# Optimization experiments

Measured on AMD Instinct MI355X. Metric: run time of the kernel, lower is better.

The kernel has to match this reference:

```python
import jax, jax.numpy as jnp
import numpy as np

BATCH = 65536
IN_FEATURES = 128
OUT_FEATURES = 128
GRID = 8  # initial_grid: number of RBF/spline basis centers per edge


def setup_inputs() -> dict:
    key = jax.random.key(0)
    k1, k2, k3 = jax.random.split(key, 3)
    x = jax.random.normal(k1, (BATCH, IN_FEATURES), dtype=jnp.float32)
    # Per-edge spline coefficients stacked: [out, in, grid]
    coeffs = jax.random.normal(k2, (OUT_FEATURES, IN_FEATURES, GRID), dtype=jnp.float32) * 0.1
    # Per-edge base (SiLU) weights stacked: [out, in]
    base_w = jax.random.normal(k3, (OUT_FEATURES, IN_FEATURES), dtype=jnp.float32) * 0.1
    # Shared uniform grid of RBF centers in [-1, 1]
    centers = jnp.linspace(-1.0, 1.0, GRID, dtype=jnp.float32)
    return {"x": x, "coeffs": coeffs, "base_w": base_w, "centers": centers}


def reference(x, coeffs, base_w, centers):
    # HybridBasisFunction per edge: base_w * silu(x) + sum_g coeffs[g] * exp(-((x-c_g)/w)^2)
    width = 2.0 / (GRID - 1)  # grid spacing
    # basis: [B, in, G]
    diff = (x[:, :, None] - centers[None, None, :]) / width
    basis = jnp.exp(-diff * diff)
    # Sum over all edges (j -> i): output[b, i] = sum_j phi_ij(x[b, j])
    out = jnp.einsum('big,oig->bo', basis, coeffs)
    out = out + jnp.einsum('bi,oi->bo', jax.nn.silu(x), base_w)
    return out
```

## Files before the change

### kernel.cpp

```cpp
#include <hip/hip_runtime.h>

typedef __fp16   pk16x2 __attribute__((ext_vector_type(2)));
typedef _Float16 f16x8  __attribute__((ext_vector_type(8)));
typedef float    f32x4  __attribute__((ext_vector_type(4)));
typedef float    f32x16 __attribute__((ext_vector_type(16)));

#define BATCH 65536
#define NIN   128
#define NOUT  128

#define L2E   1.4426950408889634f
#define SQL2E 1.2011224087864498f
#define EM2   0.1353352832366127f


__global__ __launch_bounds__(256) void kan_prep(const float* __restrict__ coeffs,
                                                const float* __restrict__ base_w,
                                                _Float16* __restrict__ W3) {
    int t = blockIdx.x * 256 + threadIdx.x;
    int ks   = t >> 8;
    int c    = t & 255;
    int nbb  = c >> 6;
    int lane = c & 63;
    int sub  = lane >> 5;
    int col  = nbb * 32 + (lane & 31);
    f16x8 v;
    if (ks < 64) {
        int g = ks >> 3, t2 = ks & 7;
        const float* src = coeffs + ((size_t)col * 128 + g * 16 + sub * 8 + t2) * 8;
#pragma unroll
        for (int e = 0; e < 8; ++e) v[e] = (_Float16)src[e];
    } else {
        const float* src = base_w + (size_t)col * 128 + (ks - 64) * 16 + sub * 8;
#pragma unroll
        for (int e = 0; e < 8; ++e) v[e] = (_Float16)src[e];
    }
    *(f16x8*)((char*)W3 + (size_t)t * 16) = v;
}

__device__ __forceinline__ void gll16(const void* g, void* l) {
    __builtin_amdgcn_global_load_lds(
        (const __attribute__((address_space(1))) unsigned int*)g,
        (__attribute__((address_space(3))) unsigned int*)l, 16, 0, 0);
}

__device__ __forceinline__ f16x8 basis8r(float t) {
    float u  = t * SQL2E;
    float b0 = __builtin_amdgcn_exp2f(-(u * u));
    float r  = __builtin_amdgcn_exp2f(__builtin_fmaf(t, 2.0f * L2E, -L2E));
    float b1 = b0 * r; r *= EM2;
    float b2 = b1 * r; r *= EM2;
    float b3 = b2 * r; r *= EM2;
    float b4 = b3 * r; r *= EM2;
    float b5 = b4 * r; r *= EM2;
    float b6 = b5 * r; r *= EM2;
    float b7 = b6 * r;
    pk16x2 p0 = __builtin_amdgcn_cvt_pkrtz(b0, b1);
    pk16x2 p1 = __builtin_amdgcn_cvt_pkrtz(b2, b3);
    pk16x2 p2 = __builtin_amdgcn_cvt_pkrtz(b4, b5);
    pk16x2 p3 = __builtin_amdgcn_cvt_pkrtz(b6, b7);
    f16x8 o;
    o[0] = p0[0]; o[1] = p0[1]; o[2] = p1[0]; o[3] = p1[1];
    o[4] = p2[0]; o[5] = p2[1]; o[6] = p3[0]; o[7] = p3[1];
    return o;
}

__device__ __forceinline__ float silu1(float xv) {
    float p = __builtin_amdgcn_exp2f(-xv * L2E);
    return xv * __builtin_amdgcn_rcpf(1.0f + p);
}

__global__ __launch_bounds__(256, 2) void kan_main(const float* __restrict__ x,
                                                   const float* __restrict__ centers,
                                                   const _Float16* __restrict__ W3,
                                                   float* __restrict__ out) {
    __shared__ _Float16 smem[2][16384];

    const int tid  = threadIdx.x;
    const int lane = tid & 63;
    const int w    = tid >> 6;
    const int l31  = lane & 31;
    const int sub  = lane >> 5;
    const int row0 = blockIdx.x * 128 + w * 32;

    const float* xp = x + (size_t)(row0 + l31) * NIN;

    f32x16 acc[4];
#pragma unroll
    for (int nbb = 0; nbb < 4; ++nbb)
#pragma unroll
        for (int r = 0; r < 16; ++r) acc[nbb][r] = 0.f;

    const char* wbase = (const char*)W3;
#define STAGE(buf, grp)                                                         \
    do {                                                                        \
        const char* _s = wbase + (size_t)(grp) * 32768 + (size_t)tid * 16;      \
        char*       _d = (char*)&smem[(buf)][0] + (size_t)tid * 16;             \
        _Pragma("unroll")                                                       \
        for (int _i = 0; _i < 8; ++_i) gll16(_s + _i * 4096, _d + _i * 4096);   \
    } while (0)

    STAGE(0, 0);
    f32x4 xa = *(const f32x4*)(xp + sub * 8);
    f32x4 xb = *(const f32x4*)(xp + sub * 8 + 4);
    __syncthreads();

#pragma unroll
    for (int g = 0; g < 8; ++g) {
        const int cur = g & 1;
        STAGE(cur ^ 1, g + 1);
        const int nxt = (g < 7) ? (g + 1) * 16 : 0;
        f32x4 xa2 = *(const f32x4*)(xp + nxt + sub * 8);
        f32x4 xb2 = *(const f32x4*)(xp + nxt + sub * 8 + 4);

        f16x8 a[8];
#pragma unroll
        for (int t2 = 0; t2 < 4; ++t2) a[t2]     = basis8r(__builtin_fmaf(xa[t2], 3.5f, 3.5f));
#pragma unroll
        for (int t2 = 0; t2 < 4; ++t2) a[4 + t2] = basis8r(__builtin_fmaf(xb[t2], 3.5f, 3.5f));

#pragma unroll
        for (int t2 = 0; t2 < 8; ++t2) {
            const char* bp = (const char*)&smem[cur][0] + t2 * 4096 + lane * 16;
#pragma unroll
            for (int nbb = 0; nbb < 4; ++nbb) {
                f16x8 b = *(const f16x8*)(bp + nbb * 1024);
                acc[nbb] = __builtin_amdgcn_mfma_f32_32x32x16_f16(a[t2], b, acc[nbb], 0, 0, 0);
            }
        }
        xa = xa2; xb = xb2;
        __syncthreads();
    }

#pragma unroll
    for (int s = 0; s < 8; ++s) {
        f32x4 xa2, xb2;
        if (s < 7) {
            xa2 = *(const f32x4*)(xp + (s + 1) * 16 + sub * 8);
            xb2 = *(const f32x4*)(xp + (s + 1) * 16 + sub * 8 + 4);
        }
        float s0 = silu1(xa[0]), s1 = silu1(xa[1]), s2 = silu1(xa[2]), s3 = silu1(xa[3]);
        float s4 = silu1(xb[0]), s5 = silu1(xb[1]), s6 = silu1(xb[2]), s7 = silu1(xb[3]);
        pk16x2 p0 = __builtin_amdgcn_cvt_pkrtz(s0, s1);
        pk16x2 p1 = __builtin_amdgcn_cvt_pkrtz(s2, s3);
        pk16x2 p2 = __builtin_amdgcn_cvt_pkrtz(s4, s5);
        pk16x2 p3 = __builtin_amdgcn_cvt_pkrtz(s6, s7);
        f16x8 a;
        a[0] = p0[0]; a[1] = p0[1]; a[2] = p1[0]; a[3] = p1[1];
        a[4] = p2[0]; a[5] = p2[1]; a[6] = p3[0]; a[7] = p3[1];
        const char* bp = (const char*)&smem[0][0] + s * 4096 + lane * 16;
#pragma unroll
        for (int nbb = 0; nbb < 4; ++nbb) {
            f16x8 b = *(const f16x8*)(bp + nbb * 1024);
            acc[nbb] = __builtin_amdgcn_mfma_f32_32x32x16_f16(a, b, acc[nbb], 0, 0, 0);
        }
        if (s < 7) { xa = xa2; xb = xb2; }
    }

#pragma unroll
    for (int nbb = 0; nbb < 4; ++nbb)
#pragma unroll
        for (int r = 0; r < 16; ++r) {
            int crow = (r & 3) + 8 * (r >> 2) + 4 * sub;
            out[(size_t)(row0 + crow) * NOUT + nbb * 32 + l31] = acc[nbb][r];
        }
}

extern "C" void kernel_launch(void* const* d_in, const int* in_sizes, int n_in,
                              void* d_out, int out_size, void* d_ws, size_t ws_size,
                              hipStream_t stream) {
    const float* x       = (const float*)d_in[0];
    const float* coeffs  = (const float*)d_in[1];
    const float* base_w  = (const float*)d_in[2];
    const float* centers = (const float*)d_in[3];
    _Float16* W3 = (_Float16*)d_ws;

    kan_prep<<<dim3(72), dim3(256), 0, stream>>>(coeffs, base_w, W3);
    kan_main<<<dim3(BATCH / 128), dim3(256), 0, stream>>>(x, centers, W3, (float*)d_out);
}
```

Measured before the change: 37.07 us.

## Keep the full per-half weight tile resident in LDS and split output columns across blocks

```diff
diff --git a/kernel.cpp b/kernel.cpp
--- a/kernel.cpp
+++ b/kernel.cpp
@@ -16,26 +16,25 @@
 
 __global__ __launch_bounds__(256) void kan_prep(const float* __restrict__ coeffs,
                                                 const float* __restrict__ base_w,
-                                                _Float16* __restrict__ W3) {
+                                                _Float16* __restrict__ W4) {
     int t = blockIdx.x * 256 + threadIdx.x;
-    int ks   = t >> 8;
-    int c    = t & 255;
-    int nbb  = c >> 6;
-    int lane = c & 63;
-    int sub  = lane >> 5;
-    int col  = nbb * 32 + (lane & 31);
+    int h    = t / 9216;
+    int rem  = t - h * 9216;
+    int kk   = rem >> 7;
+    int c2   = rem & 127;
+    int g    = kk / 9;
+    int q    = kk - g * 9;
+    int nbb2 = c2 >> 6;
+    int lane2 = c2 & 63;
+    int sub  = lane2 >> 5;
+    int col  = h * 64 + nbb2 * 32 + (lane2 & 31);
+    const float* src = (q < 8)
+        ? coeffs + ((size_t)col * 128 + g * 16 + sub * 8 + q) * 8
+        : base_w + (size_t)col * 128 + g * 16 + sub * 8;
     f16x8 v;
-    if (ks < 64) {
-        int g = ks >> 3, t2 = ks & 7;
-        const float* src = coeffs + ((size_t)col * 128 + g * 16 + sub * 8 + t2) * 8;
-#pragma unroll
-        for (int e = 0; e < 8; ++e) v[e] = (_Float16)src[e];
-    } else {
-        const float* src = base_w + (size_t)col * 128 + (ks - 64) * 16 + sub * 8;
-#pragma unroll
-        for (int e = 0; e < 8; ++e) v[e] = (_Float16)src[e];
-    }
-    *(f16x8*)((char*)W3 + (size_t)t * 16) = v;
+#pragma unroll
+    for (int e = 0; e < 8; ++e) v[e] = (_Float16)src[e];
+    *(f16x8*)((char*)W4 + (size_t)t * 16) = v;
 }
 
 __device__ __forceinline__ void gll16(const void* g, void* l) {
@@ -70,100 +69,124 @@
     return xv * __builtin_amdgcn_rcpf(1.0f + p);
 }
 
-__global__ __launch_bounds__(256, 2) void kan_main(const float* __restrict__ x,
-                                                   const float* __restrict__ centers,
-                                                   const _Float16* __restrict__ W3,
+__global__ __launch_bounds__(512, 1) void kan_main(const float* __restrict__ x,
+                                                   const _Float16* __restrict__ W4,
                                                    float* __restrict__ out) {
-    __shared__ _Float16 smem[2][16384];
+    extern __shared__ _Float16 smem[];
 
     const int tid  = threadIdx.x;
     const int lane = tid & 63;
     const int w    = tid >> 6;
     const int l31  = lane & 31;
     const int sub  = lane >> 5;
-    const int row0 = blockIdx.x * 128 + w * 32;
+    const int h    = blockIdx.x & 1;
+    const int row0 = (blockIdx.x >> 1) * 512 + w * 64;
+    const int col0 = h * 64;
+
+    const char* ws = (const char*)W4 + (size_t)h * 147456;
+    char*       ls = (char*)smem;
+#pragma unroll
+    for (int i = 0; i < 18; ++i)
+        gll16(ws + (size_t)(i * 512 + tid) * 16, ls + (size_t)(i * 512 + tid) * 16);
 
     const float* xp = x + (size_t)(row0 + l31) * NIN;
 
-    f32x16 acc[4];
-#pragma unroll
-    for (int nbb = 0; nbb < 4; ++nbb)
-#pragma unroll
-        for (int r = 0; r < 16; ++r) acc[nbb][r] = 0.f;
-
-    const char* wbase = (const char*)W3;
-#define STAGE(buf, grp)                                                         \
-    do {                                                                        \
-        const char* _s = wbase + (size_t)(grp) * 32768 + (size_t)tid * 16;      \
-        char*       _d = (char*)&smem[(buf)][0] + (size_t)tid * 16;             \
-        _Pragma("unroll")                                                       \
-        for (int _i = 0; _i < 8; ++_i) gll16(_s + _i * 4096, _d + _i * 4096);   \
+    f32x16 acc[2][2];
+#pragma unroll
+    for (int m = 0; m < 2; ++m)
+#pragma unroll
+        for (int nbb = 0; nbb < 2; ++nbb)
+#pragma unroll
+            for (int r = 0; r < 16; ++r) acc[m][nbb][r] = 0.f;
+
+    f32x4 xc00 = *(const f32x4*)(xp + sub * 8);
+    f32x4 xc01 = *(const f32x4*)(xp + sub * 8 + 4);
+    f32x4 xc10 = *(const f32x4*)(xp + 4096 + sub * 8);
+    f32x4 xc11 = *(const f32x4*)(xp + 4096 + sub * 8 + 4);
+
+    __syncthreads();
+
+#define MFMA4(A0, A1, BP)                                                        \
+    do {                                                                         \
+        f16x8 _b0 = *(const f16x8*)(BP);                                         \
+        f16x8 _b1 = *(const f16x8*)((BP) + 1024);                                \
+        acc[0][0] = __builtin_amdgcn_mfma_f32_32x32x16_f16(A0, _b0, acc[0][0], 0, 0, 0); \
+        acc[0][1] = __builtin_amdgcn_mfma_f32_32x32x16_f16(A0, _b1, acc[0][1], 0, 0, 0); \
+        acc[1][0] = __builtin_amdgcn_mfma_f32_32x32x16_f16(A1, _b0, acc[1][0], 0, 0, 0); \
+        acc[1][1] = __builtin_amdgcn_mfma_f32_32x32x16_f16(A1, _b1, acc[1][1], 0, 0, 0); \
     } while (0)
 
-    STAGE(0, 0);
-    f32x4 xa = *(const f32x4*)(xp + sub * 8);
-    f32x4 xb = *(const f32x4*)(xp + sub * 8 + 4);
-    __syncthreads();
-
 #pragma unroll
     for (int g = 0; g < 8; ++g) {
-        const int cur = g & 1;
-        STAGE(cur ^ 1, g + 1);
-        const int nxt = (g < 7) ? (g + 1) * 16 : 0;
-        f32x4 xa2 = *(const f32x4*)(xp + nxt + sub * 8);
-        f32x4 xb2 = *(const f32x4*)(xp + nxt + sub * 8 + 4);
-
-        f16x8 a[8];
-#pragma unroll
-        for (int t2 = 0; t2 < 4; ++t2) a[t2]     = basis8r(__builtin_fmaf(xa[t2], 3.5f, 3.5f));
-#pragma unroll
-        for (int t2 = 0; t2 < 4; ++t2) a[4 + t2] = basis8r(__builtin_fmaf(xb[t2], 3.5f, 3.5f));
-
-#pragma unroll
-        for (int t2 = 0; t2 < 8; ++t2) {
-            const char* bp = (const char*)&smem[cur][0] + t2 * 4096 + lane * 16;
-#pragma unroll
-            for (int nbb = 0; nbb < 4; ++nbb) {
-                f16x8 b = *(const f16x8*)(bp + nbb * 1024);
-                acc[nbb] = __builtin_amdgcn_mfma_f32_32x32x16_f16(a[t2], b, acc[nbb], 0, 0, 0);
-            }
-        }
-        xa = xa2; xb = xb2;
-        __syncthreads();
+        const int kb = g * 9;
+        f32x4 xn00, xn01, xn10, xn11;
+        if (g < 7) {
+            const float* np = xp + (g + 1) * 16 + sub * 8;
+            xn00 = *(const f32x4*)np;
+            xn01 = *(const f32x4*)(np + 4);
+            xn10 = *(const f32x4*)(np + 4096);
+            xn11 = *(const f32x4*)(np + 4100);
+        }
+        {
+            f16x8 a0[4], a1[4];
+#pragma unroll
+            for (int t2 = 0; t2 < 4; ++t2) {
+                a0[t2] = basis8r(__builtin_fmaf(xc00[t2], 3.5f, 3.5f));
+                a1[t2] = basis8r(__builtin_fmaf(xc10[t2], 3.5f, 3.5f));
+            }
+#pragma unroll
+            for (int t2 = 0; t2 < 4; ++t2) {
+                const char* bp = ls + (size_t)(kb + t2) * 2048 + lane * 16;
+                MFMA4(a0[t2], a1[t2], bp);
+            }
+        }
+        {
+            f16x8 a0[4], a1[4];
+#pragma unroll
+            for (int t2 = 0; t2 < 4; ++t2) {
+                a0[t2] = basis8r(__builtin_fmaf(xc01[t2], 3.5f, 3.5f));
+                a1[t2] = basis8r(__builtin_fmaf(xc11[t2], 3.5f, 3.5f));
+            }
+#pragma unroll
+            for (int t2 = 0; t2 < 4; ++t2) {
+                const char* bp = ls + (size_t)(kb + 4 + t2) * 2048 + lane * 16;
+                MFMA4(a0[t2], a1[t2], bp);
+            }
+        }
+        {
+            float s0 = silu1(xc00[0]), s1 = silu1(xc00[1]), s2 = silu1(xc00[2]), s3 = silu1(xc00[3]);
+            float s4 = silu1(xc01[0]), s5 = silu1(xc01[1]), s6 = silu1(xc01[2]), s7 = silu1(xc01[3]);
+            pk16x2 p0 = __builtin_amdgcn_cvt_pkrtz(s0, s1);
+            pk16x2 p1 = __builtin_amdgcn_cvt_pkrtz(s2, s3);
+            pk16x2 p2 = __builtin_amdgcn_cvt_pkrtz(s4, s5);
+            pk16x2 p3 = __builtin_amdgcn_cvt_pkrtz(s6, s7);
+            f16x8 a0;
+            a0[0] = p0[0]; a0[1] = p0[1]; a0[2] = p1[0]; a0[3] = p1[1];
+            a0[4] = p2[0]; a0[5] = p2[1]; a0[6] = p3[0]; a0[7] = p3[1];
+            float u0 = silu1(xc10[0]), u1 = silu1(xc10[1]), u2 = silu1(xc10[2]), u3 = silu1(xc10[3]);
+            float u4 = silu1(xc11[0]), u5 = silu1(xc11[1]), u6 = silu1(xc11[2]), u7 = silu1(xc11[3]);
+            pk16x2 q0 = __builtin_amdgcn_cvt_pkrtz(u0, u1);
+            pk16x2 q1 = __builtin_amdgcn_cvt_pkrtz(u2, u3);
+            pk16x2 q2 = __builtin_amdgcn_cvt_pkrtz(u4, u5);
+            pk16x2 q3 = __builtin_amdgcn_cvt_pkrtz(u6, u7);
+            f16x8 a1;
+            a1[0] = q0[0]; a1[1] = q0[1]; a1[2] = q1[0]; a1[3] = q1[1];
+            a1[4] = q2[0]; a1[5] = q2[1]; a1[6] = q3[0]; a1[7] = q3[1];
+            const char* bp = ls + (size_t)(kb + 8) * 2048 + lane * 16;
+            MFMA4(a0, a1, bp);
+        }
+        if (g < 7) { xc00 = xn00; xc01 = xn01; xc10 = xn10; xc11 = xn11; }
     }
 
 #pragma unroll
-    for (int s = 0; s < 8; ++s) {
-        f32x4 xa2, xb2;
-        if (s < 7) {
-            xa2 = *(const f32x4*)(xp + (s + 1) * 16 + sub * 8);
-            xb2 = *(const f32x4*)(xp + (s + 1) * 16 + sub * 8 + 4);
-        }
-        float s0 = silu1(xa[0]), s1 = silu1(xa[1]), s2 = silu1(xa[2]), s3 = silu1(xa[3]);
-        float s4 = silu1(xb[0]), s5 = silu1(xb[1]), s6 = silu1(xb[2]), s7 = silu1(xb[3]);
-        pk16x2 p0 = __builtin_amdgcn_cvt_pkrtz(s0, s1);
-        pk16x2 p1 = __builtin_amdgcn_cvt_pkrtz(s2, s3);
-        pk16x2 p2 = __builtin_amdgcn_cvt_pkrtz(s4, s5);
-        pk16x2 p3 = __builtin_amdgcn_cvt_pkrtz(s6, s7);
-        f16x8 a;
-        a[0] = p0[0]; a[1] = p0[1]; a[2] = p1[0]; a[3] = p1[1];
-        a[4] = p2[0]; a[5] = p2[1]; a[6] = p3[0]; a[7] = p3[1];
-        const char* bp = (const char*)&smem[0][0] + s * 4096 + lane * 16;
-#pragma unroll
-        for (int nbb = 0; nbb < 4; ++nbb) {
-            f16x8 b = *(const f16x8*)(bp + nbb * 1024);
-            acc[nbb] = __builtin_amdgcn_mfma_f32_32x32x16_f16(a, b, acc[nbb], 0, 0, 0);
-        }
-        if (s < 7) { xa = xa2; xb = xb2; }
-    }
-
-#pragma unroll
-    for (int nbb = 0; nbb < 4; ++nbb)
-#pragma unroll
-        for (int r = 0; r < 16; ++r) {
-            int crow = (r & 3) + 8 * (r >> 2) + 4 * sub;
-            out[(size_t)(row0 + crow) * NOUT + nbb * 32 + l31] = acc[nbb][r];
-        }
+    for (int m = 0; m < 2; ++m)
+#pragma unroll
+        for (int nbb = 0; nbb < 2; ++nbb)
+#pragma unroll
+            for (int r = 0; r < 16; ++r) {
+                int crow = (r & 3) + 8 * (r >> 2) + 4 * sub;
+                out[(size_t)(row0 + m * 32 + crow) * NOUT + col0 + nbb * 32 + l31] = acc[m][nbb][r];
+            }
 }
 
 extern "C" void kernel_launch(void* const* d_in, const int* in_sizes, int n_in,
@@ -172,9 +195,13 @@
     const float* x       = (const float*)d_in[0];
     const float* coeffs  = (const float*)d_in[1];
     const float* base_w  = (const float*)d_in[2];
-    const float* centers = (const float*)d_in[3];
-    _Float16* W3 = (_Float16*)d_ws;
-
-    kan_prep<<<dim3(72), dim3(256), 0, stream>>>(coeffs, base_w, W3);
-    kan_main<<<dim3(BATCH / 128), dim3(256), 0, stream>>>(x, centers, W3, (float*)d_out);
-}
+    _Float16* W4 = (_Float16*)d_ws;
+
+    static int attr_done = 0;
+    (void)attr_done;
+    hipFuncSetAttribute((const void*)kan_main,
+                        hipFuncAttributeMaxDynamicSharedMemorySize, 147456);
+
+    kan_prep<<<dim3(72), dim3(256), 0, stream>>>(coeffs, base_w, W4);
+    kan_main<<<dim3(BATCH / 256), dim3(512), 147456, stream>>>(x, W4, (float*)d_out);
+}
```

After: 40.34 us. 1.09x slower.

## Split output columns across two blocks to double grid size and occupancy

Applied to the files above, without the earlier changes.

```diff
diff --git a/kernel.cpp b/kernel.cpp
--- a/kernel.cpp
+++ b/kernel.cpp
@@ -16,26 +16,27 @@
 
 __global__ __launch_bounds__(256) void kan_prep(const float* __restrict__ coeffs,
                                                 const float* __restrict__ base_w,
-                                                _Float16* __restrict__ W3) {
+                                                _Float16* __restrict__ W5) {
     int t = blockIdx.x * 256 + threadIdx.x;
-    int ks   = t >> 8;
-    int c    = t & 255;
-    int nbb  = c >> 6;
-    int lane = c & 63;
-    int sub  = lane >> 5;
-    int col  = nbb * 32 + (lane & 31);
-    f16x8 v;
+    int h     = t / 9216;
+    int rem   = t - h * 9216;
+    int ks    = rem >> 7;
+    int c2    = rem & 127;
+    int nbb2  = c2 >> 6;
+    int lane2 = c2 & 63;
+    int sub   = lane2 >> 5;
+    int col   = h * 64 + nbb2 * 32 + (lane2 & 31);
+    const float* src;
     if (ks < 64) {
         int g = ks >> 3, t2 = ks & 7;
-        const float* src = coeffs + ((size_t)col * 128 + g * 16 + sub * 8 + t2) * 8;
+        src = coeffs + ((size_t)col * 128 + g * 16 + sub * 8 + t2) * 8;
+    } else {
+        src = base_w + (size_t)col * 128 + (ks - 64) * 16 + sub * 8;
+    }
+    f16x8 v;
 #pragma unroll
-        for (int e = 0; e < 8; ++e) v[e] = (_Float16)src[e];
-    } else {
-        const float* src = base_w + (size_t)col * 128 + (ks - 64) * 16 + sub * 8;
-#pragma unroll
-        for (int e = 0; e < 8; ++e) v[e] = (_Float16)src[e];
-    }
-    *(f16x8*)((char*)W3 + (size_t)t * 16) = v;
+    for (int e = 0; e < 8; ++e) v[e] = (_Float16)src[e];
+    *(f16x8*)((char*)W5 + (size_t)t * 16) = v;
 }
 
 __device__ __forceinline__ void gll16(const void* g, void* l) {
@@ -70,34 +71,35 @@
     return xv * __builtin_amdgcn_rcpf(1.0f + p);
 }
 
-__global__ __launch_bounds__(256, 2) void kan_main(const float* __restrict__ x,
-                                                   const float* __restrict__ centers,
-                                                   const _Float16* __restrict__ W3,
+__global__ __launch_bounds__(256, 4) void kan_main(const float* __restrict__ x,
+                                                   const _Float16* __restrict__ W5,
                                                    float* __restrict__ out) {
-    __shared__ _Float16 smem[2][16384];
+    __shared__ _Float16 smem[2][8192];
 
     const int tid  = threadIdx.x;
     const int lane = tid & 63;
     const int w    = tid >> 6;
     const int l31  = lane & 31;
     const int sub  = lane >> 5;
-    const int row0 = blockIdx.x * 128 + w * 32;
+    const int h    = blockIdx.x & 1;
+    const int row0 = (blockIdx.x >> 1) * 128 + w * 32;
+    const int col0 = h * 64;
 
     const float* xp = x + (size_t)(row0 + l31) * NIN;
 
-    f32x16 acc[4];
+    f32x16 acc[2];
 #pragma unroll
-    for (int nbb = 0; nbb < 4; ++nbb)
+    for (int nbb = 0; nbb < 2; ++nbb)
 #pragma unroll
         for (int r = 0; r < 16; ++r) acc[nbb][r] = 0.f;
 
-    const char* wbase = (const char*)W3;
+    const char* wbase = (const char*)W5 + (size_t)h * 147456;
 #define STAGE(buf, grp)                                                         \
     do {                                                                        \
-        const char* _s = wbase + (size_t)(grp) * 32768 + (size_t)tid * 16;      \
+        const char* _s = wbase + (size_t)(grp) * 16384 + (size_t)tid * 16;      \
         char*       _d = (char*)&smem[(buf)][0] + (size_t)tid * 16;             \
         _Pragma("unroll")                                                       \
-        for (int _i = 0; _i < 8; ++_i) gll16(_s + _i * 4096, _d + _i * 4096);   \
+        for (int _i = 0; _i < 4; ++_i) gll16(_s + _i * 4096, _d + _i * 4096);   \
     } while (0)
 
     STAGE(0, 0);
@@ -121,12 +123,11 @@
 
 #pragma unroll
         for (int t2 = 0; t2 < 8; ++t2) {
-            const char* bp = (const char*)&smem[cur][0] + t2 * 4096 + lane * 16;
-#pragma unroll
-            for (int nbb = 0; nbb < 4; ++nbb) {
-                f16x8 b = *(const f16x8*)(bp + nbb * 1024);
-                acc[nbb] = __builtin_amdgcn_mfma_f32_32x32x16_f16(a[t2], b, acc[nbb], 0, 0, 0);
-            }
+            const char* bp = (const char*)&smem[cur][0] + t2 * 2048 + lane * 16;
+            f16x8 b0 = *(const f16x8*)bp;
+            f16x8 b1 = *(const f16x8*)(bp + 1024);
+            acc[0] = __builtin_amdgcn_mfma_f32_32x32x16_f16(a[t2], b0, acc[0], 0, 0, 0);
+            acc[1] = __builtin_amdgcn_mfma_f32_32x32x16_f16(a[t2], b1, acc[1], 0, 0, 0);
         }
         xa = xa2; xb = xb2;
         __syncthreads();
@@ -148,21 +149,20 @@
         f16x8 a;
         a[0] = p0[0]; a[1] = p0[1]; a[2] = p1[0]; a[3] = p1[1];
         a[4] = p2[0]; a[5] = p2[1]; a[6] = p3[0]; a[7] = p3[1];
-        const char* bp = (const char*)&smem[0][0] + s * 4096 + lane * 16;
-#pragma unroll
-        for (int nbb = 0; nbb < 4; ++nbb) {
-            f16x8 b = *(const f16x8*)(bp + nbb * 1024);
-            acc[nbb] = __builtin_amdgcn_mfma_f32_32x32x16_f16(a, b, acc[nbb], 0, 0, 0);
-        }
+        const char* bp = (const char*)&smem[0][0] + s * 2048 + lane * 16;
+        f16x8 b0 = *(const f16x8*)bp;
+        f16x8 b1 = *(const f16x8*)(bp + 1024);
+        acc[0] = __builtin_amdgcn_mfma_f32_32x32x16_f16(a, b0, acc[0], 0, 0, 0);
+        acc[1] = __builtin_amdgcn_mfma_f32_32x32x16_f16(a, b1, acc[1], 0, 0, 0);
         if (s < 7) { xa = xa2; xb = xb2; }
     }
 
 #pragma unroll
-    for (int nbb = 0; nbb < 4; ++nbb)
+    for (int nbb = 0; nbb < 2; ++nbb)
 #pragma unroll
         for (int r = 0; r < 16; ++r) {
             int crow = (r & 3) + 8 * (r >> 2) + 4 * sub;
-            out[(size_t)(row0 + crow) * NOUT + nbb * 32 + l31] = acc[nbb][r];
+            out[(size_t)(row0 + crow) * NOUT + col0 + nbb * 32 + l31] = acc[nbb][r];
         }
 }
 
@@ -172,9 +172,8 @@
     const float* x       = (const float*)d_in[0];
     const float* coeffs  = (const float*)d_in[1];
     const float* base_w  = (const float*)d_in[2];
-    const float* centers = (const float*)d_in[3];
-    _Float16* W3 = (_Float16*)d_ws;
+    _Float16* W5 = (_Float16*)d_ws;
 
-    kan_prep<<<dim3(72), dim3(256), 0, stream>>>(coeffs, base_w, W3);
-    kan_main<<<dim3(BATCH / 128), dim3(256), 0, stream>>>(x, centers, W3, (float*)d_out);
+    kan_prep<<<dim3(72), dim3(256), 0, stream>>>(coeffs, base_w, W5);
+    kan_main<<<dim3(BATCH / 64), dim3(256), 0, stream>>>(x, W5, (float*)d_out);
 }
```

Result: slower. 42.91 us (+15.8%).
